# Optimization experiments

Measured on AMD Instinct MI355X. Metric: run time of the kernel, lower is better.

## Reference

```python
import jax, jax.numpy as jnp
import numpy as np

B, S, E, A = 64, 1024, 512, 128


def setup_inputs() -> dict:
    key = jax.random.key(0)
    ks = jax.random.split(key, 12)
    sc = 0.02
    states = jax.random.normal(ks[0], (B, S, E), jnp.float32)
    cls_token = jax.random.normal(ks[1], (B, E), jnp.float32)
    # ragged lengths in [2, S]; force at least one full-length row so padded width == S-1
    lengths = jax.random.randint(ks[2], (B,), 2, S + 1).at[0].set(S).astype(jnp.int32)
    position_action = (jax.random.randint(ks[3], (B,), 0, S) % (lengths - 1)).astype(jnp.int32)
    symbol_action = jax.random.randint(ks[4], (B,), 0, A).astype(jnp.int32)
    W1p = jax.random.normal(ks[5], (2 * E, 2 * E), jnp.float32) * sc
    b1p = jnp.zeros((2 * E,), jnp.float32)
    w2p = jax.random.normal(ks[6], (2 * E,), jnp.float32) * sc
    b2p = jnp.zeros((1,), jnp.float32)
    W1s = jax.random.normal(ks[7], (2 * E, 2 * E), jnp.float32) * sc
    b1s = jnp.zeros((2 * E,), jnp.float32)
    W2s = jax.random.normal(ks[8], (2 * E, A), jnp.float32) * sc
    b2s = jnp.zeros((A,), jnp.float32)
    Wc1 = jax.random.normal(ks[9], (E, E), jnp.float32) * sc
    bc1 = jnp.zeros((E,), jnp.float32)
    wc2 = jax.random.normal(ks[10], (E,), jnp.float32) * sc
    bc2 = jnp.zeros((1,), jnp.float32)
    return dict(states=states, cls_token=cls_token, W1p=W1p, b1p=b1p, w2p=w2p, b2p=b2p,
                W1s=W1s, b1s=b1s, W2s=W2s, b2s=b2s, Wc1=Wc1, bc1=bc1, wc2=wc2, bc2=bc2,
                lengths=lengths, position_action=position_action, symbol_action=symbol_action)


def reference(states, cls_token, W1p, b1p, w2p, b2p, W1s, b1s, W2s, b2s,
              Wc1, bc1, wc2, bc2, lengths, position_action, symbol_action):
    b, s, e = states.shape
    # --- get_adjacent_pairs + position_actor MLP, fused (no [.,2E] concat materialized) ---
    first, second = states[:, :-1], states[:, 1:]            # (B, S-1, E) each
    h = jax.nn.relu(jnp.einsum('bse,ef->bsf', first, W1p[:e])
                    + jnp.einsum('bse,ef->bsf', second, W1p[e:]) + b1p)  # (B, S-1, 2E)
    scores = jnp.einsum('bsf,f->bs', h, w2p) + b2p            # (B, S-1)
    # --- map_scores_to_sentences: pad invalid pair slots with -inf ---
    pos_mask = jnp.arange(s - 1)[None, :] < (lengths - 1)[:, None]
    scores = jnp.where(pos_mask, scores, -jnp.inf)
    logp = jax.nn.log_softmax(scores, axis=1)
    logp_pos = jnp.take_along_axis(logp, position_action[:, None], axis=1)[:, 0]
    logp_m = jnp.where(pos_mask, logp, 0.0)                   # safe for -inf slots
    ent_pos = -jnp.sum(jnp.exp(logp) * logp_m, axis=1)
    # --- symbol head on the pair embedding at the chosen split position ---
    bidx = jnp.arange(b)
    e1 = states[bidx, position_action]                        # (B, E)
    e2 = states[bidx, position_action + 1]                    # (B, E)
    sh = jax.nn.relu(e1 @ W1s[:e] + e2 @ W1s[e:] + b1s)       # (B, 2E)
    slogp = jax.nn.log_softmax(sh @ W2s + b2s, axis=1)        # (B, A)
    logp_sym = jnp.take_along_axis(slogp, symbol_action[:, None], axis=1)[:, 0]
    ent_sym = -jnp.sum(jnp.exp(slogp) * slogp, axis=1)
    # --- critic on cls token ---
    val = jax.nn.relu(cls_token @ Wc1 + bc1) @ wc2 + bc2      # (B,)
    return jnp.stack([logp_pos, logp_sym, val, ent_pos, ent_sym], axis=0)  # (5, B)
```

## Files before the change

kernel.cpp:

```cpp
#include <hip/hip_runtime.h>
#include <stdint.h>

#define BDIM 64
#define SDIM 1024
#define EDIM 512
#define ADIM 128
#define KDIM 1024
#define NDIM 1024

typedef unsigned short u16;
typedef __attribute__((ext_vector_type(8))) short short8;
typedef __attribute__((ext_vector_type(4))) float floatx4;
typedef const __attribute__((address_space(1))) void as1_void;
typedef __attribute__((address_space(3))) void as3_void;

__device__ inline u16 f2bf(float f){
  unsigned int u = __float_as_uint(f);
  u += 0x7fffu + ((u >> 16) & 1u);
  return (u16)(u >> 16);
}

__global__ __launch_bounds__(1024) void k_prep(
    const float* __restrict__ states,
    const float* __restrict__ W1p, const int* __restrict__ lengths,
    u16* __restrict__ sbf, u16* __restrict__ wt,
    int* __restrict__ rows, int* __restrict__ aux,
    float* __restrict__ scores)
{
  __shared__ float smem[64*65];
  const int blk = blockIdx.x, tid = threadIdx.x;

  if (blk < 1024){
    int i = blk*1024 + tid;
#pragma unroll
    for (int it = 0; it < 4; ++it, i += 1048576){
      int row = i >> 6;
      int s = row & 1023, b = row >> 10;
      if (s < lengths[b]){
        const float4* sp = (const float4*)states + (size_t)i*2;
        float4 a = sp[0], c = sp[1];
        short8 v;
        v[0]=(short)f2bf(a.x); v[1]=(short)f2bf(a.y); v[2]=(short)f2bf(a.z); v[3]=(short)f2bf(a.w);
        v[4]=(short)f2bf(c.x); v[5]=(short)f2bf(c.y); v[6]=(short)f2bf(c.z); v[7]=(short)f2bf(c.w);
        ((short8*)sbf)[i] = v;
      }
    }
    return;
  }
  if (blk < 1280){
    float (*tile)[65] = (float(*)[65])smem;
    int tb = blk - 1024;
    int zi = tb*1024 + tid;
    if (zi < 65536) scores[zi] = 0.f;
    int k0 = (tb & 15)*64, n0 = (tb >> 4)*64;
    int tx = tid & 63, ty = tid >> 6;
    for (int j = ty; j < 64; j += 16) tile[j][tx] = W1p[(size_t)(k0+j)*NDIM + n0 + tx];
    __syncthreads();
    for (int j = ty; j < 64; j += 16) wt[(size_t)(n0+j)*KDIM + k0 + tx] = f2bf(tile[tx][j]);
    return;
  }
  {
    __shared__ int scum[65];
    if (tid == 0){
      int c = 0;
      for (int b = 0; b < 64; ++b){ scum[b] = c; c += lengths[b] - 1; }
      scum[64] = c;
    }
    __syncthreads();
    if (tid < 65) aux[tid] = scum[tid];
    if (tid == 0){
      aux[70] = scum[64];
      aux[71] = (scum[64] + 127) >> 7;
    }
    for (int b = 0; b < 64; ++b){
      int base = scum[b], L = scum[b+1] - scum[b];
      for (int i2 = tid; i2 < L; i2 += 1024) rows[base + i2] = (b << 10) + i2;
    }
  }
}

__global__ __launch_bounds__(256, 2) void k_gemm_scores(
    const u16* __restrict__ sbf, const u16* __restrict__ wt,
    const float* __restrict__ b1p, const float* __restrict__ w2p,
    const int* __restrict__ rows, const int* __restrict__ aux,
    float* __restrict__ scores,
    const float* __restrict__ states, const float* __restrict__ cls,
    const float* __restrict__ W1s, const float* __restrict__ b1s,
    const float* __restrict__ Wc1, const float* __restrict__ bc1,
    const float* __restrict__ wc2, const float* __restrict__ bc2,
    const int* __restrict__ pos_action,
    float* __restrict__ sh, float* __restrict__ out)
{
  __shared__ short8 LDS[2048];
  const int tid = threadIdx.x;
  const int j = blockIdx.x;

  if (j < 256){
    float* xs = (float*)LDS;
    int b = j >> 2, n0 = (j & 3) * 256;
    int pa = pos_action[b];
    const float* src = states + (size_t)(b*SDIM + pa) * EDIM;
    xs[tid]       = src[tid];
    xs[tid + 256] = src[tid + 256];
    xs[tid + 512] = src[tid + 512];
    xs[tid + 768] = src[tid + 768];
    __syncthreads();
    int n = n0 + tid;
    float acc = 0.f;
#pragma unroll 8
    for (int k = 0; k < 1024; ++k)
      acc = fmaf(xs[k], W1s[(size_t)k*1024 + n], acc);
    sh[b*1024 + n] = fmaxf(acc + b1s[n], 0.f);
    return;
  }
  if (j < 320){
    float* xs = (float*)LDS;
    float* r2 = (float*)LDS + 512;
    int b = j - 256;
    xs[tid]       = cls[b*EDIM + tid];
    xs[tid + 256] = cls[b*EDIM + tid + 256];
    __syncthreads();
    float a0 = 0.f, a1 = 0.f;
#pragma unroll 8
    for (int k = 0; k < 512; ++k){
      float x = xs[k];
      a0 = fmaf(x, Wc1[(size_t)k*EDIM + tid],       a0);
      a1 = fmaf(x, Wc1[(size_t)k*EDIM + tid + 256], a1);
    }
    float p = fmaxf(a0 + bc1[tid],       0.f) * wc2[tid]
            + fmaxf(a1 + bc1[tid + 256], 0.f) * wc2[tid + 256];
    for (int off = 32; off; off >>= 1) p += __shfl_xor(p, off);
    if ((tid & 63) == 0) r2[tid >> 6] = p;
    __syncthreads();
    if (tid == 0) out[128 + b] = bc2[0] + r2[0] + r2[1] + r2[2] + r2[3];
    return;
  }

  short8* Ash = LDS;
  short8* Bsh = LDS + 1024;
  const int w = tid >> 6, l = tid & 63;
  const int jg = j - 320;
  const int tl = ((jg >> 6) << 3) | (jg & 7);
  const int nt = (jg >> 3) & 7;
  const int total = aux[70];
  if (tl >= aux[71]) return;

  const int lrow8 = l >> 3;
  const int c = (l & 7) ^ lrow8;
  const char* sbase = (const char*)sbf;
  const char* wbase = (const char*)wt;
  int offA[4], offB[4];
#pragma unroll
  for (int i = 0; i < 4; ++i){
    int mloc = (w*4 + i)*8 + lrow8;
    int mg = tl*128 + mloc;
    if (mg >= total) mg = 0;
    int rs = rows[mg];
    offA[i] = rs*1024 + c*16;
    int nloc = (w*4 + i)*8 + lrow8;
    offB[i] = (nt*128 + nloc)*2048 + c*16;
  }

  const int r = l & 15, q = l >> 4;
  const int wm = w & 1, wn = w >> 1;
  int aIdx[4], bIdx[4];
#pragma unroll
  for (int i = 0; i < 4; ++i){
    int m = wm*64 + i*16 + r;
    aIdx[i] = m*8 + (q ^ (r & 7));
    int n = wn*64 + i*16 + r;
    bIdx[i] = n*8 + (q ^ (r & 7));
  }

  floatx4 acc[4][4];
#pragma unroll
  for (int a = 0; a < 4; ++a)
#pragma unroll
    for (int b = 0; b < 4; ++b) acc[a][b] = (floatx4)(0.0f);

  for (int step = 0; step < 16; ++step){
    const int ktb = step * 128;
    __syncthreads();
#pragma unroll
    for (int i = 0; i < 4; ++i){
      __builtin_amdgcn_global_load_lds((as1_void*)(sbase + offA[i] + ktb),
                                       (as3_void*)((char*)Ash + (w*4 + i)*1024), 16, 0, 0);
    }
#pragma unroll
    for (int i = 0; i < 4; ++i){
      __builtin_amdgcn_global_load_lds((as1_void*)(wbase + offB[i] + ktb),
                                       (as3_void*)((char*)Bsh + (w*4 + i)*1024), 16, 0, 0);
    }
    __syncthreads();
#pragma unroll
    for (int kh = 0; kh < 2; ++kh){
      short8 af[4], bf[4];
#pragma unroll
      for (int i = 0; i < 4; ++i) af[i] = Ash[aIdx[i] ^ (kh*4)];
#pragma unroll
      for (int i = 0; i < 4; ++i) bf[i] = Bsh[bIdx[i] ^ (kh*4)];
#pragma unroll
      for (int mi = 0; mi < 4; ++mi)
#pragma unroll
        for (int ni = 0; ni < 4; ++ni)
          acc[mi][ni] = __builtin_amdgcn_mfma_f32_16x16x32_bf16(af[mi], bf[ni], acc[mi][ni], 0, 0, 0);
    }
  }

  const int mrow0 = tl*128 + wm*64;
  const int ncol0 = nt*128 + wn*64;
#pragma unroll
  for (int mi = 0; mi < 4; ++mi){
    float t0 = 0.f, t1 = 0.f, t2 = 0.f, t3 = 0.f;
#pragma unroll
    for (int ni = 0; ni < 4; ++ni){
      int n = ncol0 + ni*16 + r;
      float bb = b1p[n], ww = w2p[n];
      floatx4 a = acc[mi][ni];
      t0 += fmaxf(a[0] + bb, 0.f) * ww;
      t1 += fmaxf(a[1] + bb, 0.f) * ww;
      t2 += fmaxf(a[2] + bb, 0.f) * ww;
      t3 += fmaxf(a[3] + bb, 0.f) * ww;
    }
#pragma unroll
    for (int off = 1; off < 16; off <<= 1){
      t0 += __shfl_xor(t0, off);
      t1 += __shfl_xor(t1, off);
      t2 += __shfl_xor(t2, off);
      t3 += __shfl_xor(t3, off);
    }
    if (r == 0){
      int row = mrow0 + mi*16 + q*4;
      if (row + 0 < total) atomicAdd(&scores[row + 0], t0);
      if (row + 1 < total) atomicAdd(&scores[row + 1], t1);
      if (row + 2 < total) atomicAdd(&scores[row + 2], t2);
      if (row + 3 < total) atomicAdd(&scores[row + 3], t3);
    }
  }
}

__global__ __launch_bounds__(1024) void k_post(
    const float* __restrict__ scores, const float* __restrict__ sh,
    const float* __restrict__ W2s, const float* __restrict__ b2s,
    const int* __restrict__ aux, const int* __restrict__ lengths,
    const int* __restrict__ pos_action, const int* __restrict__ sym_action,
    float* __restrict__ out)
{
  __shared__ float smem[2208];
  const int blk = blockIdx.x, tid = threadIdx.x;
  if (blk < 64){
    float* sc   = smem;
    float* red  = smem + 1024;
    float* red2 = smem + 1040;
    int b = blk;
    int L = lengths[b] - 1;
    const float* sp = scores + aux[b];
    float mx = -1e30f;
    for (int s = tid; s < L; s += 1024){
      float v = sp[s];
      sc[s] = v;
      mx = fmaxf(mx, v);
    }
    for (int off = 32; off; off >>= 1) mx = fmaxf(mx, __shfl_xor(mx, off));
    if ((tid & 63) == 0) red[tid >> 6] = mx;
    __syncthreads();
    mx = -1e30f;
#pragma unroll
    for (int jj = 0; jj < 16; ++jj) mx = fmaxf(mx, red[jj]);
    float se = 0.f, ses = 0.f;
    for (int s = tid; s < L; s += 1024){
      float v = sc[s];
      float e = expf(v - mx);
      se += e; ses += e * v;
    }
    for (int off = 32; off; off >>= 1){ se += __shfl_xor(se, off); ses += __shfl_xor(ses, off); }
    __syncthreads();
    if ((tid & 63) == 0){ red[tid >> 6] = se; red2[tid >> 6] = ses; }
    __syncthreads();
    if (tid == 0){
      float S = 0.f, SS = 0.f;
#pragma unroll
      for (int jj = 0; jj < 16; ++jj){ S += red[jj]; SS += red2[jj]; }
      float logZ = logf(S);
      int pa = pos_action[b];
      out[b]       = sc[pa] - mx - logZ;
      out[192 + b] = mx + logZ - SS / S;
    }
    return;
  }
  {
    float* xs  = smem;
    float* red = smem + 1024;
    float* lg  = smem + 2048;
    float* r2  = smem + 2176;
    float* r3  = smem + 2192;
    int b = blk - 64;
    xs[tid] = sh[b*1024 + tid];
    __syncthreads();
    int n = tid & 127;
    int f0 = (tid >> 7) * 128;
    float acc = 0.f;
#pragma unroll 8
    for (int jj = 0; jj < 128; ++jj){
      int f = f0 + jj;
      acc = fmaf(xs[f], W2s[(size_t)f*ADIM + n], acc);
    }
    red[tid] = acc;
    __syncthreads();
    if (tid < 128){
      float s = b2s[tid];
#pragma unroll
      for (int jj = 0; jj < 8; ++jj) s += red[tid + jj*128];
      lg[tid] = s;
    }
    __syncthreads();
    float v = (tid < 128) ? lg[tid] : -1e30f;
    float mx = v;
    for (int off = 32; off; off >>= 1) mx = fmaxf(mx, __shfl_xor(mx, off));
    if ((tid & 63) == 0) r2[tid >> 6] = mx;
    __syncthreads();
    mx = -1e30f;
#pragma unroll
    for (int jj = 0; jj < 16; ++jj) mx = fmaxf(mx, r2[jj]);
    float e = (tid < 128) ? expf(v - mx) : 0.f;
    float se = e, ses = (tid < 128) ? e * v : 0.f;
    for (int off = 32; off; off >>= 1){ se += __shfl_xor(se, off); ses += __shfl_xor(ses, off); }
    __syncthreads();
    if ((tid & 63) == 0){ r2[tid >> 6] = se; r3[tid >> 6] = ses; }
    __syncthreads();
    if (tid == 0){
      float S = 0.f, SS = 0.f;
#pragma unroll
      for (int jj = 0; jj < 16; ++jj){ S += r2[jj]; SS += r3[jj]; }
      float logZ = logf(S);
      out[64 + b]  = lg[sym_action[b]] - mx - logZ;
      out[256 + b] = mx + logZ - SS / S;
    }
  }
}

extern "C" void kernel_launch(void* const* d_in, const int* in_sizes, int n_in,
                              void* d_out, int out_size, void* d_ws, size_t ws_size,
                              hipStream_t stream){
  const float* states = (const float*)d_in[0];
  const float* cls    = (const float*)d_in[1];
  const float* W1p    = (const float*)d_in[2];
  const float* b1p    = (const float*)d_in[3];
  const float* w2p    = (const float*)d_in[4];
  const float* W1s    = (const float*)d_in[6];
  const float* b1s    = (const float*)d_in[7];
  const float* W2s    = (const float*)d_in[8];
  const float* b2s    = (const float*)d_in[9];
  const float* Wc1    = (const float*)d_in[10];
  const float* bc1    = (const float*)d_in[11];
  const float* wc2    = (const float*)d_in[12];
  const float* bc2    = (const float*)d_in[13];
  const int* lengths  = (const int*)d_in[14];
  const int* pos_a    = (const int*)d_in[15];
  const int* sym_a    = (const int*)d_in[16];
  float* out = (float*)d_out;

  char* ws = (char*)d_ws;
  u16* sbf      = (u16*)ws;
  u16* wt       = (u16*)(ws + 67108864);
  float* scores = (float*)(ws + 69206016);
  float* sh     = (float*)(ws + 69468160);
  int* rows     = (int*)(ws + 69730304);
  int* aux      = (int*)(ws + 69992448);

  k_prep<<<1281, 1024, 0, stream>>>(states, W1p, lengths, sbf, wt, rows, aux, scores);
  k_gemm_scores<<<4416, 256, 0, stream>>>(sbf, wt, b1p, w2p, rows, aux, scores,
                                          states, cls, W1s, b1s, Wc1, bc1, wc2, bc2,
                                          pos_a, sh, out);
  k_post<<<128, 1024, 0, stream>>>(scores, sh, W2s, b2s, aux, lengths, pos_a, sym_a, out);
}
```

Before: 317.3 us.

## Compute symbol-head hidden layer with bf16 MFMA tiles instead of scalar FMA

The symbol-head hidden layer (64 gathered pair rows times W1s) was computed by 256 blocks doing scalar fp32 FMA loops. It now runs in 8 blocks that each use bf16 MFMA over a 64x128 output tile. The gathered A rows come from the already-converted bf16 states buffer, indexed through extra row entries written in k_prep, and W1s is converted to bf16 on the fly. This cuts the grid size and the scalar work, at the cost of bf16 precision in this head and a heavier per-block workload.

Measured after the change: 303.7 us. 1.04x faster.

```diff
diff --git a/kernel.cpp b/kernel.cpp
--- a/kernel.cpp
+++ b/kernel.cpp
@@ -23,6 +23,7 @@
 __global__ __launch_bounds__(1024) void k_prep(
     const float* __restrict__ states,
     const float* __restrict__ W1p, const int* __restrict__ lengths,
+    const int* __restrict__ pos_action,
     u16* __restrict__ sbf, u16* __restrict__ wt,
     int* __restrict__ rows, int* __restrict__ aux,
     float* __restrict__ scores)
@@ -72,6 +73,7 @@
       aux[70] = scum[64];
       aux[71] = (scum[64] + 127) >> 7;
     }
+    if (tid < 64) rows[65472 + tid] = (tid << 10) + pos_action[tid];
     for (int b = 0; b < 64; ++b){
       int base = scum[b], L = scum[b+1] - scum[b];
       for (int i2 = tid; i2 < L; i2 += 1024) rows[base + i2] = (b << 10) + i2;
@@ -84,39 +86,103 @@
     const float* __restrict__ b1p, const float* __restrict__ w2p,
     const int* __restrict__ rows, const int* __restrict__ aux,
     float* __restrict__ scores,
-    const float* __restrict__ states, const float* __restrict__ cls,
+    const float* __restrict__ cls,
     const float* __restrict__ W1s, const float* __restrict__ b1s,
     const float* __restrict__ Wc1, const float* __restrict__ bc1,
     const float* __restrict__ wc2, const float* __restrict__ bc2,
-    const int* __restrict__ pos_action,
     float* __restrict__ sh, float* __restrict__ out)
 {
   __shared__ short8 LDS[2048];
   const int tid = threadIdx.x;
   const int j = blockIdx.x;
 
-  if (j < 256){
-    float* xs = (float*)LDS;
-    int b = j >> 2, n0 = (j & 3) * 256;
-    int pa = pos_action[b];
-    const float* src = states + (size_t)(b*SDIM + pa) * EDIM;
-    xs[tid]       = src[tid];
-    xs[tid + 256] = src[tid + 256];
-    xs[tid + 512] = src[tid + 512];
-    xs[tid + 768] = src[tid + 768];
-    __syncthreads();
-    int n = n0 + tid;
-    float acc = 0.f;
-#pragma unroll 8
-    for (int k = 0; k < 1024; ++k)
-      acc = fmaf(xs[k], W1s[(size_t)k*1024 + n], acc);
-    sh[b*1024 + n] = fmaxf(acc + b1s[n], 0.f);
+  if (j < 8){
+    short8* Ash = LDS;
+    short8* Bsh = LDS + 512;
+    const int w = tid >> 6, l = tid & 63;
+    const int n0 = j * 128;
+    const int lrow8 = l >> 3;
+    const int c = (l & 7) ^ lrow8;
+    const char* sbase = (const char*)sbf;
+    int offA[2];
+#pragma unroll
+    for (int i = 0; i < 2; ++i){
+      int mloc = (w*2 + i)*8 + lrow8;
+      int rs = rows[65472 + mloc];
+      offA[i] = rs*1024 + c*16;
+    }
+    const int r = l & 15, q = l >> 4;
+    const int wm = w & 1, wn = w >> 1;
+    int aIdx[2], bIdx[4];
+#pragma unroll
+    for (int i = 0; i < 2; ++i){
+      int m = wm*32 + i*16 + r;
+      aIdx[i] = m*8 + (q ^ (r & 7));
+    }
+#pragma unroll
+    for (int i = 0; i < 4; ++i){
+      int n = wn*64 + i*16 + r;
+      bIdx[i] = n*8 + (q ^ (r & 7));
+    }
+    const int kt8 = tid >> 5, nq = tid & 31;
+    floatx4 acc[2][4];
+#pragma unroll
+    for (int a = 0; a < 2; ++a)
+#pragma unroll
+      for (int b = 0; b < 4; ++b) acc[a][b] = (floatx4)(0.0f);
+
+    for (int step = 0; step < 16; ++step){
+      __syncthreads();
+#pragma unroll
+      for (int i = 0; i < 2; ++i)
+        __builtin_amdgcn_global_load_lds((as1_void*)(sbase + offA[i] + step*128),
+                                         (as3_void*)((char*)Ash + (w*2 + i)*1024), 16, 0, 0);
+      const float* wsrc = W1s + (size_t)(step*64 + kt8*8)*1024 + n0 + nq*4;
+      float v[8][4];
+#pragma unroll
+      for (int kk = 0; kk < 8; ++kk)
+        *(float4*)v[kk] = *(const float4*)(wsrc + (size_t)kk*1024);
+#pragma unroll
+      for (int jj = 0; jj < 4; ++jj){
+        short8 c8;
+#pragma unroll
+        for (int kk = 0; kk < 8; ++kk) c8[kk] = (short)f2bf(v[kk][jj]);
+        int R = nq*4 + jj;
+        Bsh[R*8 + (kt8 ^ (R & 7))] = c8;
+      }
+      __syncthreads();
+#pragma unroll
+      for (int kh = 0; kh < 2; ++kh){
+        short8 af[2], bf[4];
+#pragma unroll
+        for (int i = 0; i < 2; ++i) af[i] = Ash[aIdx[i] ^ (kh*4)];
+#pragma unroll
+        for (int i = 0; i < 4; ++i) bf[i] = Bsh[bIdx[i] ^ (kh*4)];
+#pragma unroll
+        for (int mi = 0; mi < 2; ++mi)
+#pragma unroll
+          for (int ni = 0; ni < 4; ++ni)
+            acc[mi][ni] = __builtin_amdgcn_mfma_f32_16x16x32_bf16(af[mi], bf[ni], acc[mi][ni], 0, 0, 0);
+      }
+    }
+#pragma unroll
+    for (int mi = 0; mi < 2; ++mi)
+#pragma unroll
+      for (int ni = 0; ni < 4; ++ni){
+        int row = wm*32 + mi*16 + q*4;
+        int col = n0 + wn*64 + ni*16 + r;
+        floatx4 a = acc[mi][ni];
+        float bb = b1s[col];
+#pragma unroll
+        for (int jj = 0; jj < 4; ++jj)
+          sh[(row + jj)*1024 + col] = fmaxf(a[jj] + bb, 0.f);
+      }
     return;
   }
-  if (j < 320){
+  if (j < 72){
     float* xs = (float*)LDS;
     float* r2 = (float*)LDS + 512;
-    int b = j - 256;
+    int b = j - 8;
     xs[tid]       = cls[b*EDIM + tid];
     xs[tid + 256] = cls[b*EDIM + tid + 256];
     __syncthreads();
@@ -139,7 +205,7 @@
   short8* Ash = LDS;
   short8* Bsh = LDS + 1024;
   const int w = tid >> 6, l = tid & 63;
-  const int jg = j - 320;
+  const int jg = j - 72;
   const int tl = ((jg >> 6) << 3) | (jg & 7);
   const int nt = (jg >> 3) & 7;
   const int total = aux[70];
@@ -368,9 +434,8 @@
   int* rows     = (int*)(ws + 69730304);
   int* aux      = (int*)(ws + 69992448);
 
-  k_prep<<<1281, 1024, 0, stream>>>(states, W1p, lengths, sbf, wt, rows, aux, scores);
-  k_gemm_scores<<<4416, 256, 0, stream>>>(sbf, wt, b1p, w2p, rows, aux, scores,
-                                          states, cls, W1s, b1s, Wc1, bc1, wc2, bc2,
-                                          pos_a, sh, out);
+  k_prep<<<1281, 1024, 0, stream>>>(states, W1p, lengths, pos_a, sbf, wt, rows, aux, scores);
+  k_gemm_scores<<<4168, 256, 0, stream>>>(sbf, wt, b1p, w2p, rows, aux, scores,
+                                          cls, W1s, b1s, Wc1, bc1, wc2, bc2, sh, out);
   k_post<<<128, 1024, 0, stream>>>(scores, sh, W2s, b2s, aux, lengths, pos_a, sym_a, out);
 }
```
